# Kernel optimization log

Measured on AMD Instinct MI355X. Metric: run time of the kernel, lower is better.

Reference implementation:

```python
import jax, jax.numpy as jnp
import numpy as np

B, T, C = 2, 2048, 1024
N_HEAD = 16
G_NON = 32   # qgroup_size_non (layernorm / residual path)
G_LIN = 32   # qgroup_size_lin (linear path)
QMAX = 127.0
EPS = 1e-5


def quantize(x, G):
    """Group-wise symmetric int8 quantization along the last dim.
    Returns q (int8, same shape as x) and scales s with shape x.shape[:-1] + (D//G,)."""
    shp = x.shape
    xg = x.reshape(shp[:-1] + (shp[-1] // G, G))
    s = jnp.maximum(jnp.max(jnp.abs(xg), axis=-1) / QMAX, 1e-8)
    q = jnp.clip(jnp.round(xg / s[..., None]), -QMAX, QMAX).astype(jnp.int8)
    return q.reshape(shp), s


def dequant(q, s, G):
    shp = q.shape
    xg = q.astype(jnp.float32).reshape(shp[:-1] + (shp[-1] // G, G)) * s[..., None]
    return xg.reshape(shp)


def quant_dequant(x, G):
    """Fake-quantize (straight-through): forward = dequant(quantize(x))."""
    q, s = quantize(x, G)
    xd = dequant(q, s, G)
    return x + jax.lax.stop_gradient(xd - x)


def setup_inputs() -> dict:
    key = jax.random.key(0)
    k1, k2, k3, k4 = jax.random.split(key, 4)
    x = jax.random.normal(k1, (B, T, C), dtype=jnp.float32)
    # LN stats of x, produced by the previous block's int8_add_..._MeanVar
    mean = jnp.mean(x, axis=-1)
    rstd = 1.0 / jnp.sqrt(jnp.var(x, axis=-1) + EPS)
    qx, sx = quantize(x, G_NON)
    ln_w = 1.0 + 0.02 * jax.random.normal(k2, (C,), dtype=jnp.float32)
    w1 = 0.02 * jax.random.normal(k3, (3 * C, C), dtype=jnp.float32)   # c_attn.weight [out,in]
    w2 = 0.02 * jax.random.normal(k4, (C, C), dtype=jnp.float32)       # c_proj.weight [out,in]
    return {"x": x, "qx": qx.astype(jnp.int32), "sx": sx, "mean": mean,
            "rstd": rstd, "ln_w": ln_w, "w1": w1, "w2": w2}


def reference(x, qx, sx, mean, rstd, ln_w, w1, w2):
    hd = C // N_HEAD
    # ---- Part1: int8 layernorm (uses provided mean/rstd) + int8 c_attn linear ----
    ln_in = dequant(qx.astype(jnp.int8), sx, G_NON)               # [B,T,C]
    h = (ln_in - mean[..., None]) * rstd[..., None] * ln_w        # layernorm output
    hq = quant_dequant(h, G_NON)                                  # requantize activations
    w1q = quant_dequant(w1, G_LIN)                                # int8 weight
    qkv = jnp.einsum('btc,oc->bto', hq, w1q)                      # [B,T,3C]
    q, k, v = jnp.split(qkv, 3, axis=-1)
    q = q.reshape(B, T, N_HEAD, hd).transpose(0, 2, 1, 3)         # [B,H,T,hd]
    k = k.reshape(B, T, N_HEAD, hd).transpose(0, 2, 1, 3)
    v = v.reshape(B, T, N_HEAD, hd).transpose(0, 2, 1, 3)
    # ---- causal SDPA ----
    scores = jnp.einsum('bhqd,bhkd->bhqk', q, k) / jnp.sqrt(jnp.float32(hd))
    causal = jnp.tril(jnp.ones((T, T), dtype=bool))
    scores = jnp.where(causal, scores, jnp.float32(-1e30))
    attn = jax.nn.softmax(scores, axis=-1)
    y = jnp.einsum('bhqk,bhkd->bhqd', attn, v)
    y = y.transpose(0, 2, 1, 3).reshape(B, T, C)
    # ---- Part2: int8 c_proj linear + residual add with mean/var ----
    yq = quant_dequant(y, G_LIN)
    w2q = quant_dequant(w2, G_LIN)
    proj = jnp.einsum('btc,oc->bto', yq, w2q)
    fpx = x + proj                                                # fp residual output
    mean_o = jnp.mean(fpx, axis=-1)
    rstd_o = 1.0 / jnp.sqrt(jnp.var(fpx, axis=-1) + EPS)
    qo, so = quantize(fpx, G_NON)                                 # quantized output for next block
    return (fpx, qo, so, mean_o, rstd_o)
```

## Files before the change

### kernel.cpp

```cpp
#include <hip/hip_runtime.h>
#include <stdint.h>

#define BB 2
#define TT 2048
#define CC 1024
#define NH 16
#define HD 64
#define NG 32
#define ROWS (BB*TT)
#define C3 (3*CC)

typedef _Float16 half_t;
typedef __attribute__((ext_vector_type(8))) _Float16 half8;
typedef __attribute__((ext_vector_type(2))) __fp16 fp16x2;
typedef __attribute__((ext_vector_type(4))) float f32x4;
typedef __attribute__((ext_vector_type(16))) float f32x16;

#define GLDS16(g, l) __builtin_amdgcn_global_load_lds( \
    (__attribute__((address_space(1))) void*)(g), \
    (__attribute__((address_space(3))) void*)(l), 16, 0, 0)

#define LOG2E 1.44269504f
#define DEFER_THR 5.5451774f

__device__ __forceinline__ uint32_t pk_h2(float a, float b) {
  union { fp16x2 h; uint32_t u; } cv;
  cv.h = __builtin_amdgcn_cvt_pkrtz(a, b);
  return cv.u;
}

__global__ void k_qdq_w(const float* __restrict__ w1, const float* __restrict__ w2,
                        half_t* __restrict__ o1, half_t* __restrict__ o2) {
  int g = blockIdx.x * blockDim.x + threadIdx.x;
  const float* src; half_t* dst; int gl;
  if (g < C3 * NG) { src = w1; dst = o1; gl = g; }
  else             { src = w2; dst = o2; gl = g - C3 * NG; }
  const float4* p = reinterpret_cast<const float4*>(src + (size_t)gl * 32);
  float v[32]; float amax = 0.f;
  #pragma unroll
  for (int i = 0; i < 8; ++i) {
    float4 t = p[i];
    v[4*i] = t.x; v[4*i+1] = t.y; v[4*i+2] = t.z; v[4*i+3] = t.w;
    amax = fmaxf(amax, fmaxf(fmaxf(fabsf(t.x), fabsf(t.y)), fmaxf(fabsf(t.z), fabsf(t.w))));
  }
  float s = fmaxf(amax / 127.0f, 1e-8f);
  half_t* o = dst + (size_t)gl * 32;
  #pragma unroll
  for (int c = 0; c < 4; ++c) {
    half8 ov;
    #pragma unroll
    for (int jj = 0; jj < 8; ++jj) {
      float q = fminf(fmaxf(rintf(v[c*8+jj] / s), -127.f), 127.f);
      ov[jj] = (half_t)(q * s);
    }
    *reinterpret_cast<half8*>(o + c*8) = ov;
  }
}

__global__ void k_qh(const int* __restrict__ qx, const float* __restrict__ sx,
                     const float* __restrict__ mean, const float* __restrict__ rstd,
                     const float* __restrict__ lnw, half_t* __restrict__ h16) {
  int g = blockIdx.x * blockDim.x + threadIdx.x;
  if (g >= ROWS * NG) return;
  int row = g >> 5, grp = g & 31;
  float sxv = sx[g];
  float mu = mean[row], rs = rstd[row];
  const int4* qp = reinterpret_cast<const int4*>(qx + (size_t)row * CC + grp * 32);
  const float4* wp = reinterpret_cast<const float4*>(lnw + grp * 32);
  float v[32]; float amax = 0.f;
  #pragma unroll
  for (int i = 0; i < 8; ++i) {
    int4 qv = qp[i]; float4 wv = wp[i];
    float h0 = ((float)qv.x * sxv - mu) * rs * wv.x;
    float h1 = ((float)qv.y * sxv - mu) * rs * wv.y;
    float h2 = ((float)qv.z * sxv - mu) * rs * wv.z;
    float h3 = ((float)qv.w * sxv - mu) * rs * wv.w;
    v[4*i] = h0; v[4*i+1] = h1; v[4*i+2] = h2; v[4*i+3] = h3;
    amax = fmaxf(amax, fmaxf(fmaxf(fabsf(h0), fabsf(h1)), fmaxf(fabsf(h2), fabsf(h3))));
  }
  float s = fmaxf(amax / 127.0f, 1e-8f);
  half_t* o = h16 + (size_t)row * CC + grp * 32;
  #pragma unroll
  for (int c = 0; c < 4; ++c) {
    half8 ov;
    #pragma unroll
    for (int jj = 0; jj < 8; ++jj) {
      float q = fminf(fmaxf(rintf(v[c*8+jj] / s), -127.f), 127.f);
      ov[jj] = (half_t)(q * s);
    }
    *reinterpret_cast<half8*>(o + c*8) = ov;
  }
}

template<typename TO>
__global__ __launch_bounds__(256) void k_gemm16(const half_t* __restrict__ A,
                                                const half_t* __restrict__ B,
                                                TO* __restrict__ Out, int N,
                                                int gx, int cpx, int klen) {
  __shared__ __align__(16) half_t As[2][128*32];
  __shared__ __align__(16) half_t Bs[2][128*32];
  const int tid = threadIdx.x;
  const int wave = tid >> 6, lane = tid & 63;
  const int l15 = lane & 15, lg = lane >> 4;
  const int flat = blockIdx.y * gx + blockIdx.x;
  const int swz = (flat & 7) * cpx + (flat >> 3);
  const int m0 = (swz / gx) * 128, n0 = (swz % gx) * 128;
  const int kbeg = blockIdx.z * klen;
  TO* out = Out + (size_t)blockIdx.z * ROWS * N;
  const int wm = (wave >> 1) * 64, wn = (wave & 1) * 64;
  f32x4 acc[4][4];
  #pragma unroll
  for (int i = 0; i < 4; ++i)
    #pragma unroll
    for (int jj = 0; jj < 4; ++jj) acc[i][jj] = f32x4{0.f, 0.f, 0.f, 0.f};
  const int srow = lane >> 2;
  const int scol = (lane & 3) * 8;
  const int seg0 = wave * 2;
  auto stage = [&](int buf, int k0) {
    #pragma unroll
    for (int s = 0; s < 2; ++s) {
      const int seg = seg0 + s;
      GLDS16(A + (size_t)(m0 + seg*16 + srow) * 1024 + k0 + scol, &As[buf][0] + seg*512);
      GLDS16(B + (size_t)(n0 + seg*16 + srow) * 1024 + k0 + scol, &Bs[buf][0] + seg*512);
    }
  };
  stage(0, kbeg);
  __syncthreads();
  int cur = 0;
  for (int k0 = kbeg; k0 < kbeg + klen; k0 += 32) {
    if (k0 + 32 < kbeg + klen) stage(cur ^ 1, k0 + 32);
    half8 af[4], bf[4];
    #pragma unroll
    for (int i = 0; i < 4; ++i) {
      af[i] = *reinterpret_cast<const half8*>(&As[cur][0] + (wm + i*16 + l15)*32 + lg*8);
      bf[i] = *reinterpret_cast<const half8*>(&Bs[cur][0] + (wn + i*16 + l15)*32 + lg*8);
    }
    #pragma unroll
    for (int mi = 0; mi < 4; ++mi)
      #pragma unroll
      for (int ni = 0; ni < 4; ++ni)
        acc[mi][ni] = __builtin_amdgcn_mfma_f32_16x16x32_f16(af[mi], bf[ni], acc[mi][ni], 0, 0, 0);
    __syncthreads();
    cur ^= 1;
  }
  const int crow = m0 + wm + lg * 4;
  const int ccol = n0 + wn + l15;
  #pragma unroll
  for (int mi = 0; mi < 4; ++mi)
    #pragma unroll
    for (int ni = 0; ni < 4; ++ni)
      #pragma unroll
      for (int r = 0; r < 4; ++r)
        out[(size_t)(crow + mi*16 + r) * N + ccol + ni*16] = (TO)acc[mi][ni][r];
}

__global__ __launch_bounds__(512, 4) void k_attn32(const half_t* __restrict__ qkv,
                                                   half_t* __restrict__ y16) {
  __shared__ __align__(16) half_t smem[4][64*72];
  const int tid = threadIdx.x;
  const int wave = tid >> 6, lane = tid & 63;
  const int l31 = lane & 31, lh = lane >> 5;
  const int bh = blockIdx.x, b = bh >> 4, h = bh & 15;
  const int j = blockIdx.y;
  const int tile = wave >> 2, par = (wave >> 1) & 1, rh = wave & 1;
  const int qt = tile ? (31 - j) : j;
  const int ktmax = 31 - j;

  const size_t qrow = (size_t)(b * TT + qt * 64 + rh * 32 + l31);
  const half_t* qp = qkv + qrow * C3 + h * HD + lh * 8;
  half8 qreg[4];
  #pragma unroll
  for (int kk = 0; kk < 4; ++kk)
    qreg[kk] = *reinterpret_cast<const half8*>(qp + kk * 16) * (half_t)0.125f;

  float m = -3.0e38f, lsum = 0.f;
  f32x16 yacc[2];
  yacc[0] = (f32x16)(0.f); yacc[1] = (f32x16)(0.f);

  const int sj = tid >> 3, sc = (tid & 7) * 8;
  const int vkp = tid >> 4, vd0 = (tid & 15) * 4;
  const int csp = (vkp & 0x19) | ((vkp & 2) << 1) | ((vkp & 4) >> 1);
  const int vxor = ((vd0 >> 3) & 7) << 2;

  int vbase[2], vxr[2];
  #pragma unroll
  for (int db = 0; db < 2; ++db) {
    const int d = db * 32 + l31;
    vbase[db] = d * 36 + lh * 4;
    vxr[db] = ((d >> 3) & 7) << 2;
  }

  half8 k0r; uint2 u0r, u1r;
  const half_t* kvb = qkv + ((size_t)b * TT) * C3 + CC + h * HD;
  auto kload = [&](int kt) {
    const half_t* kp = kvb + (size_t)(kt*64 + sj) * C3 + sc;
    k0r = *reinterpret_cast<const half8*>(kp);
    const half_t* vp = kvb + (size_t)(kt*64 + vkp*2) * C3 + CC + vd0;
    u0r = *reinterpret_cast<const uint2*>(vp);
    u1r = *reinterpret_cast<const uint2*>(vp + C3);
  };
  auto stage = [&](int buf) {
    *reinterpret_cast<half8*>(&smem[buf][0] + sj*72 + sc) = k0r;
    uint32_t* vt32 = reinterpret_cast<uint32_t*>(&smem[2 + buf][0]);
    vt32[(((vd0+0)*36 + csp)) ^ vxor] = __builtin_amdgcn_perm(u1r.x, u0r.x, 0x05040100u);
    vt32[(((vd0+1)*36 + csp)) ^ vxor] = __builtin_amdgcn_perm(u1r.x, u0r.x, 0x07060302u);
    vt32[(((vd0+2)*36 + csp)) ^ vxor] = __builtin_amdgcn_perm(u1r.y, u0r.y, 0x05040100u);
    vt32[(((vd0+3)*36 + csp)) ^ vxor] = __builtin_amdgcn_perm(u1r.y, u0r.y, 0x07060302u);
  };

  kload(0);
  stage(0);
  kload(1);
  __syncthreads();
  for (int kt = 0; kt <= ktmax; ++kt) {
    const int cur = kt & 1;
    if (kt < ktmax) {
      stage(cur ^ 1);
      if (kt + 2 <= ktmax) kload(kt + 2);
    }
    if (((kt & 1) == par) && kt <= qt) {
      const half_t* ksb = &smem[cur][0];
      const uint32_t* vt32 = reinterpret_cast<const uint32_t*>(&smem[2 + cur][0]);
      f32x16 sacc[2];
      sacc[0] = (f32x16)(0.f); sacc[1] = (f32x16)(0.f);
      __builtin_amdgcn_s_setprio(1);
      #pragma unroll
      for (int kb = 0; kb < 2; ++kb)
        #pragma unroll
        for (int kk = 0; kk < 4; ++kk) {
          const half8 a = *reinterpret_cast<const half8*>(
              ksb + (kb*32 + l31)*72 + kk*16 + lh*8);
          sacc[kb] = __builtin_amdgcn_mfma_f32_32x32x16_f16(a, qreg[kk], sacc[kb], 0, 0, 0);
        }
      __builtin_amdgcn_s_setprio(0);
      float sv[2][16]; float tm = -3.0e38f;
      const bool diag = (kt == qt);
      const int qloc = rh * 32 + l31;
      #pragma unroll
      for (int kb = 0; kb < 2; ++kb)
        #pragma unroll
        for (int r = 0; r < 16; ++r) {
          float s = sacc[kb][r];
          if (diag && (kb*32 + (r&3) + 8*(r>>2) + 4*lh > qloc)) s = -1e30f;
          sv[kb][r] = s;
          tm = fmaxf(tm, s);
        }
      tm = fmaxf(tm, __shfl_xor(tm, 32));
      if (!__all(tm <= m + DEFER_THR)) {
        const float mn = fmaxf(m, tm);
        const float alpha = __builtin_amdgcn_exp2f((m - mn) * LOG2E);
        yacc[0] *= alpha; yacc[1] *= alpha;
        lsum *= alpha;
        m = mn;
      }
      const float nm = -m * LOG2E;
      float rs = 0.f;
      #pragma unroll
      for (int kb = 0; kb < 2; ++kb)
        #pragma unroll
        for (int r = 0; r < 16; ++r) {
          sv[kb][r] = __builtin_amdgcn_exp2f(fmaf(sv[kb][r], LOG2E, nm));
          rs += sv[kb][r];
        }
      lsum += rs;
      uint32_t w[2][8];
      #pragma unroll
      for (int kb = 0; kb < 2; ++kb)
        #pragma unroll
        for (int r2 = 0; r2 < 8; ++r2)
          w[kb][r2] = pk_h2(sv[kb][2*r2], sv[kb][2*r2+1]);
      __builtin_amdgcn_s_setprio(1);
      #pragma unroll
      for (int db = 0; db < 2; ++db)
        #pragma unroll
        for (int kb = 0; kb < 2; ++kb)
          #pragma unroll
          for (int kk = 0; kk < 2; ++kk) {
            const int gdw = (vbase[db] + kb*16 + kk*8) ^ vxr[db];
            const half8 va = *reinterpret_cast<const half8*>(vt32 + gdw);
            union { uint32_t u[4]; half8 h; } bf;
            bf.u[0] = w[kb][4*kk + 0]; bf.u[1] = w[kb][4*kk + 1];
            bf.u[2] = w[kb][4*kk + 2]; bf.u[3] = w[kb][4*kk + 3];
            yacc[db] = __builtin_amdgcn_mfma_f32_32x32x16_f16(va, bf.h, yacc[db], 0, 0, 0);
          }
      __builtin_amdgcn_s_setprio(0);
    }
    __syncthreads();
  }

  float* mb = reinterpret_cast<float*>(&smem[0][0]);
  const int pr = tile * 2 + rh;
  float* yb = mb + pr * 2176;
  if (par == 0) {
    #pragma unroll
    for (int db = 0; db < 2; ++db)
      #pragma unroll
      for (int r = 0; r < 16; ++r)
        yb[(db*16 + r) * 64 + lane] = yacc[db][r];
    yb[2048 + lane] = m;
    yb[2112 + lane] = lsum;
  }
  __syncthreads();
  if (par == 1) {
    const float me = yb[2048 + lane];
    const float le = yb[2112 + lane];
    const float M = fmaxf(m, me);
    const float ae = __builtin_amdgcn_exp2f((me - M) * LOG2E);
    const float ao = __builtin_amdgcn_exp2f((m - M) * LOG2E);
    float lt = le * ae + lsum * ao;
    lt += __shfl_xor(lt, 32);
    const float inv = 1.0f / lt;
    float yv[2][16];
    #pragma unroll
    for (int db = 0; db < 2; ++db)
      #pragma unroll
      for (int r = 0; r < 16; ++r)
        yv[db][r] = (yb[(db*16 + r) * 64 + lane] * ae + yacc[db][r] * ao) * inv;
    half_t* yp = y16 + qrow * CC + h * HD;
    #pragma unroll
    for (int db = 0; db < 2; ++db) {
      float am = 0.f;
      #pragma unroll
      for (int r = 0; r < 16; ++r) am = fmaxf(am, fabsf(yv[db][r]));
      am = fmaxf(am, __shfl_xor(am, 32));
      const float s = fmaxf(am / 127.0f, 1e-8f);
      const float qi = 1.0f / s;
      #pragma unroll
      for (int t = 0; t < 4; ++t) {
        union { half_t h4[4]; uint64_t u; } pk;
        #pragma unroll
        for (int rr = 0; rr < 4; ++rr) {
          float q = fminf(fmaxf(rintf(yv[db][4*t + rr] * qi), -127.f), 127.f);
          pk.h4[rr] = (half_t)(q * s);
        }
        *reinterpret_cast<uint64_t*>(yp + db*32 + 8*t + 4*lh) = pk.u;
      }
    }
  }
}

__global__ __launch_bounds__(256) void k_final(
    const float* __restrict__ x, const half_t* __restrict__ p0,
    const half_t* __restrict__ p1,
    float* __restrict__ out_fpx, float* __restrict__ out_qo, float* __restrict__ out_so,
    float* __restrict__ out_mean, float* __restrict__ out_rstd) {
  __shared__ float red[16];
  int row = blockIdx.x;
  int tid = threadIdx.x;
  size_t base = (size_t)row * CC + tid * 4;
  float4 xv = *reinterpret_cast<const float4*>(x + base);
  union { uint64_t u; half_t h[4]; } pa, pb;
  pa.u = *reinterpret_cast<const uint64_t*>(p0 + base);
  pb.u = *reinterpret_cast<const uint64_t*>(p1 + base);
  float4 f;
  f.x = xv.x + (float)pa.h[0] + (float)pb.h[0];
  f.y = xv.y + (float)pa.h[1] + (float)pb.h[1];
  f.z = xv.z + (float)pa.h[2] + (float)pb.h[2];
  f.w = xv.w + (float)pa.h[3] + (float)pb.h[3];
  *reinterpret_cast<float4*>(out_fpx + base) = f;
  float sum = f.x + f.y + f.z + f.w;
  float sq  = f.x*f.x + f.y*f.y + f.z*f.z + f.w*f.w;
  #pragma unroll
  for (int off = 1; off < 64; off <<= 1) {
    sum += __shfl_xor(sum, off);
    sq  += __shfl_xor(sq, off);
  }
  int wid = tid >> 6, lane = tid & 63;
  if (lane == 0) { red[wid] = sum; red[8 + wid] = sq; }
  __syncthreads();
  if (tid == 0) {
    float s4 = red[0] + red[1] + red[2] + red[3];
    float q4 = red[8] + red[9] + red[10] + red[11];
    float mu = s4 * (1.0f / CC);
    float var = q4 * (1.0f / CC) - mu * mu;
    out_mean[row] = mu;
    out_rstd[row] = 1.0f / sqrtf(var + 1e-5f);
  }
  float amax = fmaxf(fmaxf(fabsf(f.x), fabsf(f.y)), fmaxf(fabsf(f.z), fabsf(f.w)));
  #pragma unroll
  for (int off = 1; off < 8; off <<= 1) amax = fmaxf(amax, __shfl_xor(amax, off, 8));
  float s = fmaxf(amax / 127.0f, 1e-8f);
  int g = tid >> 3, li = tid & 7;
  if (li == 0) out_so[row * NG + g] = s;
  float4 qo;
  qo.x = fminf(fmaxf(rintf(f.x / s), -127.f), 127.f);
  qo.y = fminf(fmaxf(rintf(f.y / s), -127.f), 127.f);
  qo.z = fminf(fmaxf(rintf(f.z / s), -127.f), 127.f);
  qo.w = fminf(fmaxf(rintf(f.w / s), -127.f), 127.f);
  *reinterpret_cast<float4*>(out_qo + base) = qo;
}

extern "C" void kernel_launch(void* const* d_in, const int* in_sizes, int n_in,
                              void* d_out, int out_size, void* d_ws, size_t ws_size,
                              hipStream_t stream) {
  const float* x    = (const float*)d_in[0];
  const int*   qx   = (const int*)d_in[1];
  const float* sx   = (const float*)d_in[2];
  const float* mean = (const float*)d_in[3];
  const float* rstd = (const float*)d_in[4];
  const float* lnw  = (const float*)d_in[5];
  const float* w1   = (const float*)d_in[6];
  const float* w2   = (const float*)d_in[7];

  float* out = (float*)d_out;
  float* o_fpx  = out;
  float* o_qo   = o_fpx + (size_t)ROWS * CC;
  float* o_so   = o_qo  + (size_t)ROWS * CC;
  float* o_mean = o_so  + (size_t)ROWS * NG;
  float* o_rstd = o_mean + ROWS;

  size_t off = 0;
  char* wsb = (char*)d_ws;
  auto alloc = [&](size_t bytes) -> void* {
    void* p = wsb + off;
    off += (bytes + 255) & ~(size_t)255;
    return p;
  };
  half_t* h16   = (half_t*)alloc((size_t)ROWS * CC * 2);
  half_t* w116  = (half_t*)alloc((size_t)C3 * CC * 2);
  half_t* w216  = (half_t*)alloc((size_t)CC * CC * 2);
  half_t* qkv16 = (half_t*)alloc((size_t)ROWS * C3 * 2);
  half_t* y16   = (half_t*)alloc((size_t)ROWS * CC * 2);
  half_t* proj  = (half_t*)alloc((size_t)2 * ROWS * CC * 2);

  k_qdq_w<<<(C3 * NG + CC * NG) / 256, 256, 0, stream>>>(w1, w2, w116, w216);
  k_qh<<<(ROWS * NG) / 256, 256, 0, stream>>>(qx, sx, mean, rstd, lnw, h16);
  k_gemm16<half_t><<<dim3(C3 / 128, ROWS / 128, 1), 256, 0, stream>>>(
      h16, w116, qkv16, C3, C3 / 128, (C3 / 128) * (ROWS / 128) / 8, 1024);
  k_attn32<<<dim3(BB * NH, 16), 512, 0, stream>>>(qkv16, y16);
  k_gemm16<half_t><<<dim3(CC / 128, ROWS / 128, 2), 256, 0, stream>>>(
      y16, w216, proj, CC, CC / 128, (CC / 128) * (ROWS / 128) / 8, 512);
  k_final<<<ROWS, 256, 0, stream>>>(x, proj, proj + (size_t)ROWS * CC,
                                    o_fpx, o_qo, o_so, o_mean, o_rstd);
}
```

Baseline: 141.1 us.

## Balance causal attention work across four wave-pair splits with multi-way merge

The attention kernel now splits the key tiles of the two paired query tiles (j and 31-j) into four contiguous ranges, assigned to four wave pairs with a 1/2/3-way split chosen to minimize the longest range. Each group of 128 threads stages its own K/V tile into a private LDS slot using wider 16-byte loads. A multi-way softmax merge through LDS combines the partial results. This replaces the earlier even/odd interleave with shared staging, and is meant to reduce idle waves and load imbalance. In exchange it uses more LDS per block, more registers for the wider loads, and a longer merge epilogue.

```diff
diff --git a/kernel.cpp b/kernel.cpp
--- a/kernel.cpp
+++ b/kernel.cpp
@@ -156,17 +156,38 @@
 
 __global__ __launch_bounds__(512, 4) void k_attn32(const half_t* __restrict__ qkv,
                                                    half_t* __restrict__ y16) {
-  __shared__ __align__(16) half_t smem[4][64*72];
+  __shared__ __align__(16) half_t smem[4 * 2 * 4608];
   const int tid = threadIdx.x;
   const int wave = tid >> 6, lane = tid & 63;
   const int l31 = lane & 31, lh = lane >> 5;
   const int bh = blockIdx.x, b = bh >> 4, h = bh & 15;
   const int j = blockIdx.y;
-  const int tile = wave >> 2, par = (wave >> 1) & 1, rh = wave & 1;
-  const int qt = tile ? (31 - j) : j;
-  const int ktmax = 31 - j;
-
-  const size_t qrow = (size_t)(b * TT + qt * 64 + rh * 32 + l31);
+  const int nA = j + 1, nB = 32 - j;
+
+  int kA = 1, maxlen = 1 << 30;
+  #pragma unroll
+  for (int k = 1; k <= 3; ++k) {
+    const int l1 = (nA + k - 1) / k;
+    const int l2 = (nB + (3 - k)) / (4 - k);
+    const int mx = l1 > l2 ? l1 : l2;
+    if (mx < maxlen) { maxlen = mx; kA = k; }
+  }
+  auto sdesc = [&](int s, int& base, int& len, int& sqt) {
+    const int tB = (s >= kA);
+    const int n = tB ? nB : nA;
+    const int k = tB ? (4 - kA) : kA;
+    const int i = tB ? (s - kA) : s;
+    const int q = n / k, r = n % k;
+    base = i * q + (i < r ? i : r);
+    len = q + (i < r ? 1 : 0);
+    sqt = tB ? (31 - j) : j;
+  };
+
+  const int sid = wave >> 1, rh = wave & 1;
+  int wbase, wlen, wqt;
+  sdesc(sid, wbase, wlen, wqt);
+
+  const size_t qrow = (size_t)(b * TT + wqt * 64 + rh * 32 + l31);
   const half_t* qp = qkv + qrow * C3 + h * HD + lh * 8;
   half8 qreg[4];
   #pragma unroll
@@ -176,11 +197,6 @@
   float m = -3.0e38f, lsum = 0.f;
   f32x16 yacc[2];
   yacc[0] = (f32x16)(0.f); yacc[1] = (f32x16)(0.f);
-
-  const int sj = tid >> 3, sc = (tid & 7) * 8;
-  const int vkp = tid >> 4, vd0 = (tid & 15) * 4;
-  const int csp = (vkp & 0x19) | ((vkp & 2) << 1) | ((vkp & 4) >> 1);
-  const int vxor = ((vd0 >> 3) & 7) << 2;
 
   int vbase[2], vxr[2];
   #pragma unroll
@@ -190,37 +206,55 @@
     vxr[db] = ((d >> 3) & 7) << 2;
   }
 
-  half8 k0r; uint2 u0r, u1r;
+  const int g = tid >> 7, t128 = tid & 127;
+  int gbase, glen, gqt_;
+  sdesc(g, gbase, glen, gqt_);
+  const int skey = t128 >> 1, sch = (t128 & 1) * 32;
+  const int vkp = t128 >> 2, vd0 = (t128 & 3) * 16;
+  const int csp = (vkp & 0x19) | ((vkp & 2) << 1) | ((vkp & 4) >> 1);
+
+  uint4 kr0, kr1, kr2, kr3, v0a, v0b, v1a, v1b;
   const half_t* kvb = qkv + ((size_t)b * TT) * C3 + CC + h * HD;
   auto kload = [&](int kt) {
-    const half_t* kp = kvb + (size_t)(kt*64 + sj) * C3 + sc;
-    k0r = *reinterpret_cast<const half8*>(kp);
+    const half_t* kp = kvb + (size_t)(kt*64 + skey) * C3 + sch;
+    kr0 = *reinterpret_cast<const uint4*>(kp);
+    kr1 = *reinterpret_cast<const uint4*>(kp + 8);
+    kr2 = *reinterpret_cast<const uint4*>(kp + 16);
+    kr3 = *reinterpret_cast<const uint4*>(kp + 24);
     const half_t* vp = kvb + (size_t)(kt*64 + vkp*2) * C3 + CC + vd0;
-    u0r = *reinterpret_cast<const uint2*>(vp);
-    u1r = *reinterpret_cast<const uint2*>(vp + C3);
+    v0a = *reinterpret_cast<const uint4*>(vp);
+    v0b = *reinterpret_cast<const uint4*>(vp + 8);
+    v1a = *reinterpret_cast<const uint4*>(vp + C3);
+    v1b = *reinterpret_cast<const uint4*>(vp + C3 + 8);
   };
-  auto stage = [&](int buf) {
-    *reinterpret_cast<half8*>(&smem[buf][0] + sj*72 + sc) = k0r;
-    uint32_t* vt32 = reinterpret_cast<uint32_t*>(&smem[2 + buf][0]);
-    vt32[(((vd0+0)*36 + csp)) ^ vxor] = __builtin_amdgcn_perm(u1r.x, u0r.x, 0x05040100u);
-    vt32[(((vd0+1)*36 + csp)) ^ vxor] = __builtin_amdgcn_perm(u1r.x, u0r.x, 0x07060302u);
-    vt32[(((vd0+2)*36 + csp)) ^ vxor] = __builtin_amdgcn_perm(u1r.y, u0r.y, 0x05040100u);
-    vt32[(((vd0+3)*36 + csp)) ^ vxor] = __builtin_amdgcn_perm(u1r.y, u0r.y, 0x07060302u);
+  auto stage = [&]() {
+    half_t* ks = smem + g * 9216;
+    *reinterpret_cast<uint4*>(ks + skey*72 + sch)      = kr0;
+    *reinterpret_cast<uint4*>(ks + skey*72 + sch + 8)  = kr1;
+    *reinterpret_cast<uint4*>(ks + skey*72 + sch + 16) = kr2;
+    *reinterpret_cast<uint4*>(ks + skey*72 + sch + 24) = kr3;
+    uint32_t* vt = reinterpret_cast<uint32_t*>(ks + 4608);
+    const uint32_t w0[8] = {v0a.x, v0a.y, v0a.z, v0a.w, v0b.x, v0b.y, v0b.z, v0b.w};
+    const uint32_t w1[8] = {v1a.x, v1a.y, v1a.z, v1a.w, v1b.x, v1b.y, v1b.z, v1b.w};
+    #pragma unroll
+    for (int i = 0; i < 8; ++i) {
+      const int d = vd0 + 2*i;
+      const int x = ((d >> 3) & 7) << 2;
+      vt[(d*36 + csp) ^ x]       = __builtin_amdgcn_perm(w1[i], w0[i], 0x05040100u);
+      vt[((d+1)*36 + csp) ^ x]   = __builtin_amdgcn_perm(w1[i], w0[i], 0x07060302u);
+    }
   };
 
-  kload(0);
-  stage(0);
-  kload(1);
-  __syncthreads();
-  for (int kt = 0; kt <= ktmax; ++kt) {
-    const int cur = kt & 1;
-    if (kt < ktmax) {
-      stage(cur ^ 1);
-      if (kt + 2 <= ktmax) kload(kt + 2);
-    }
-    if (((kt & 1) == par) && kt <= qt) {
-      const half_t* ksb = &smem[cur][0];
-      const uint32_t* vt32 = reinterpret_cast<const uint32_t*>(&smem[2 + cur][0]);
+  kload(gbase);
+  for (int t = 0; t < maxlen; ++t) {
+    __syncthreads();
+    if (t < glen) stage();
+    __syncthreads();
+    if (t + 1 < glen) kload(gbase + t + 1);
+    if (t < wlen) {
+      const int kt = wbase + t;
+      const half_t* ksb = smem + sid * 9216;
+      const uint32_t* vt32 = reinterpret_cast<const uint32_t*>(ksb + 4608);
       f32x16 sacc[2];
       sacc[0] = (f32x16)(0.f); sacc[1] = (f32x16)(0.f);
       __builtin_amdgcn_s_setprio(1);
@@ -234,7 +268,7 @@
         }
       __builtin_amdgcn_s_setprio(0);
       float sv[2][16]; float tm = -3.0e38f;
-      const bool diag = (kt == qt);
+      const bool diag = (kt == wqt);
       const int qloc = rh * 32 + l31;
       #pragma unroll
       for (int kb = 0; kb < 2; ++kb)
@@ -285,37 +319,49 @@
           }
       __builtin_amdgcn_s_setprio(0);
     }
-    __syncthreads();
-  }
-
-  float* mb = reinterpret_cast<float*>(&smem[0][0]);
-  const int pr = tile * 2 + rh;
-  float* yb = mb + pr * 2176;
-  if (par == 0) {
+  }
+
+  __syncthreads();
+  float* mb = reinterpret_cast<float*>(smem);
+  float* yb = mb + wave * 2176;
+  #pragma unroll
+  for (int db = 0; db < 2; ++db)
+    #pragma unroll
+    for (int r = 0; r < 16; ++r)
+      yb[(db*16 + r) * 64 + lane] = yacc[db][r];
+  yb[2048 + lane] = m;
+  yb[2112 + lane] = lsum;
+  __syncthreads();
+  const bool ismg = (sid == 0) || (sid == kA);
+  if (ismg) {
+    const int s0 = (sid == 0) ? 0 : kA;
+    const int sn = (sid == 0) ? kA : (4 - kA);
+    float M = m;
+    for (int s = 1; s < sn; ++s)
+      M = fmaxf(M, mb[((s0 + s)*2 + rh)*2176 + 2048 + lane]);
+    const float a0 = __builtin_amdgcn_exp2f((m - M) * LOG2E);
+    float lh_ = lsum * a0;
+    float yv[2][16];
     #pragma unroll
     for (int db = 0; db < 2; ++db)
       #pragma unroll
-      for (int r = 0; r < 16; ++r)
-        yb[(db*16 + r) * 64 + lane] = yacc[db][r];
-    yb[2048 + lane] = m;
-    yb[2112 + lane] = lsum;
-  }
-  __syncthreads();
-  if (par == 1) {
-    const float me = yb[2048 + lane];
-    const float le = yb[2112 + lane];
-    const float M = fmaxf(m, me);
-    const float ae = __builtin_amdgcn_exp2f((me - M) * LOG2E);
-    const float ao = __builtin_amdgcn_exp2f((m - M) * LOG2E);
-    float lt = le * ae + lsum * ao;
-    lt += __shfl_xor(lt, 32);
+      for (int r = 0; r < 16; ++r) yv[db][r] = yacc[db][r] * a0;
+    for (int s = 1; s < sn; ++s) {
+      float* pb = mb + ((s0 + s)*2 + rh)*2176;
+      const float as = __builtin_amdgcn_exp2f((pb[2048 + lane] - M) * LOG2E);
+      lh_ += pb[2112 + lane] * as;
+      #pragma unroll
+      for (int db = 0; db < 2; ++db)
+        #pragma unroll
+        for (int r = 0; r < 16; ++r)
+          yv[db][r] += pb[(db*16 + r) * 64 + lane] * as;
+    }
+    float lt = lh_ + __shfl_xor(lh_, 32);
     const float inv = 1.0f / lt;
-    float yv[2][16];
     #pragma unroll
     for (int db = 0; db < 2; ++db)
       #pragma unroll
-      for (int r = 0; r < 16; ++r)
-        yv[db][r] = (yb[(db*16 + r) * 64 + lane] * ae + yacc[db][r] * ao) * inv;
+      for (int r = 0; r < 16; ++r) yv[db][r] *= inv;
     half_t* yp = y16 + qrow * CC + h * HD;
     #pragma unroll
     for (int db = 0; db < 2; ++db) {
```

Measured after the change: 207.8 us. 1.47x slower.

## Stage two KV tiles per barrier epoch, one per half-block, in attention

Applied to the files above, without the earlier changes.

The attention kernel's K/V staging loop now processes two key tiles per iteration, one per half of the block, instead of one tile per iteration with half the waves idle. Each half of the threads loads and stages its own tile using wider 16-byte loads. Shared memory becomes four K+V buffers in a double-buffered pair. This halves the number of loop iterations and barriers, so both wave parities compute in the same epoch. In exchange, each thread holds more registers for the loaded K/V data, and the per-thread V transpose indexing changes.

```diff
diff --git a/kernel.cpp b/kernel.cpp
--- a/kernel.cpp
+++ b/kernel.cpp
@@ -156,7 +156,7 @@
 
 __global__ __launch_bounds__(512, 4) void k_attn32(const half_t* __restrict__ qkv,
                                                    half_t* __restrict__ y16) {
-  __shared__ __align__(16) half_t smem[4][64*72];
+  __shared__ __align__(16) half_t smem[4][9216];
   const int tid = threadIdx.x;
   const int wave = tid >> 6, lane = tid & 63;
   const int l31 = lane & 31, lh = lane >> 5;
@@ -165,6 +165,7 @@
   const int tile = wave >> 2, par = (wave >> 1) & 1, rh = wave & 1;
   const int qt = tile ? (31 - j) : j;
   const int ktmax = 31 - j;
+  const int E = (ktmax >> 1) + 1;
 
   const size_t qrow = (size_t)(b * TT + qt * 64 + rh * 32 + l31);
   const half_t* qp = qkv + qrow * C3 + h * HD + lh * 8;
@@ -176,11 +177,6 @@
   float m = -3.0e38f, lsum = 0.f;
   f32x16 yacc[2];
   yacc[0] = (f32x16)(0.f); yacc[1] = (f32x16)(0.f);
-
-  const int sj = tid >> 3, sc = (tid & 7) * 8;
-  const int vkp = tid >> 4, vd0 = (tid & 15) * 4;
-  const int csp = (vkp & 0x19) | ((vkp & 2) << 1) | ((vkp & 4) >> 1);
-  const int vxor = ((vd0 >> 3) & 7) << 2;
 
   int vbase[2], vxr[2];
   #pragma unroll
@@ -190,37 +186,51 @@
     vxr[db] = ((d >> 3) & 7) << 2;
   }
 
-  half8 k0r; uint2 u0r, u1r;
+  const int ts = tid >> 8, t256 = tid & 255;
+  const int skey = t256 >> 2, sch = (t256 & 3) * 16;
+  const int vkp = t256 >> 3, vd0 = (t256 & 7) * 8;
+  const int csp = (vkp & 0x19) | ((vkp & 2) << 1) | ((vkp & 4) >> 1);
+
+  uint4 kr0, kr1, v0r, v1r;
   const half_t* kvb = qkv + ((size_t)b * TT) * C3 + CC + h * HD;
   auto kload = [&](int kt) {
-    const half_t* kp = kvb + (size_t)(kt*64 + sj) * C3 + sc;
-    k0r = *reinterpret_cast<const half8*>(kp);
+    const half_t* kp = kvb + (size_t)(kt*64 + skey) * C3 + sch;
+    kr0 = *reinterpret_cast<const uint4*>(kp);
+    kr1 = *reinterpret_cast<const uint4*>(kp + 8);
     const half_t* vp = kvb + (size_t)(kt*64 + vkp*2) * C3 + CC + vd0;
-    u0r = *reinterpret_cast<const uint2*>(vp);
-    u1r = *reinterpret_cast<const uint2*>(vp + C3);
+    v0r = *reinterpret_cast<const uint4*>(vp);
+    v1r = *reinterpret_cast<const uint4*>(vp + C3);
   };
   auto stage = [&](int buf) {
-    *reinterpret_cast<half8*>(&smem[buf][0] + sj*72 + sc) = k0r;
-    uint32_t* vt32 = reinterpret_cast<uint32_t*>(&smem[2 + buf][0]);
-    vt32[(((vd0+0)*36 + csp)) ^ vxor] = __builtin_amdgcn_perm(u1r.x, u0r.x, 0x05040100u);
-    vt32[(((vd0+1)*36 + csp)) ^ vxor] = __builtin_amdgcn_perm(u1r.x, u0r.x, 0x07060302u);
-    vt32[(((vd0+2)*36 + csp)) ^ vxor] = __builtin_amdgcn_perm(u1r.y, u0r.y, 0x05040100u);
-    vt32[(((vd0+3)*36 + csp)) ^ vxor] = __builtin_amdgcn_perm(u1r.y, u0r.y, 0x07060302u);
+    half_t* ks = &smem[buf][0];
+    *reinterpret_cast<uint4*>(ks + skey*72 + sch)     = kr0;
+    *reinterpret_cast<uint4*>(ks + skey*72 + sch + 8) = kr1;
+    uint32_t* vt = reinterpret_cast<uint32_t*>(ks + 4608);
+    const uint32_t w0[4] = {v0r.x, v0r.y, v0r.z, v0r.w};
+    const uint32_t w1[4] = {v1r.x, v1r.y, v1r.z, v1r.w};
+    #pragma unroll
+    for (int i = 0; i < 4; ++i) {
+      const int d = vd0 + 2*i;
+      const int x = ((d >> 3) & 7) << 2;
+      vt[(d*36 + csp) ^ x]     = __builtin_amdgcn_perm(w1[i], w0[i], 0x05040100u);
+      vt[((d+1)*36 + csp) ^ x] = __builtin_amdgcn_perm(w1[i], w0[i], 0x07060302u);
+    }
   };
 
-  kload(0);
-  stage(0);
-  kload(1);
+  kload(ts);
+  stage(ts);
+  if (2 + ts <= ktmax) kload(2 + ts);
   __syncthreads();
-  for (int kt = 0; kt <= ktmax; ++kt) {
-    const int cur = kt & 1;
-    if (kt < ktmax) {
-      stage(cur ^ 1);
-      if (kt + 2 <= ktmax) kload(kt + 2);
-    }
-    if (((kt & 1) == par) && kt <= qt) {
-      const half_t* ksb = &smem[cur][0];
-      const uint32_t* vt32 = reinterpret_cast<const uint32_t*>(&smem[2 + cur][0]);
+
+  for (int e = 0; e < E; ++e) {
+    if (e + 1 < E && 2*(e+1) + ts <= ktmax) {
+      stage(((e+1) & 1) * 2 + ts);
+      if (e + 2 < E && 2*(e+2) + ts <= ktmax) kload(2*(e+2) + ts);
+    }
+    const int kt = 2*e + par;
+    if (kt <= qt) {
+      const half_t* ksb = &smem[(e & 1) * 2 + par][0];
+      const uint32_t* vt32 = reinterpret_cast<const uint32_t*>(ksb + 4608);
       f32x16 sacc[2];
       sacc[0] = (f32x16)(0.f); sacc[1] = (f32x16)(0.f);
       __builtin_amdgcn_s_setprio(1);
```

Result: slower. 156.8 us (+11.2%).
